# Performance work log

Measured on AMD Instinct MI355X. Metric: run time of the kernel, lower is better.

## Reference

```python
import jax, jax.numpy as jnp
import numpy as np

N_NODES = 50000
N_EDGES = 800000
N_LABELS = 50      # len(deplabel2idx) == len(deplabels)
EMB = 64           # dep_emb_size
HID = 96           # dep_hidden_dim


def _glorot(key, shape):
    fan_in, fan_out = shape
    lim = jnp.sqrt(6.0 / (fan_in + fan_out)).astype(jnp.float32)
    return jax.random.uniform(key, shape, jnp.float32, -lim, lim)


def setup_inputs() -> dict:
    key = jax.random.key(0)
    ks = jax.random.split(key, 10)
    dep_labels = jax.random.randint(ks[0], (N_NODES,), 0, N_LABELS)
    src = jax.random.randint(ks[1], (N_EDGES,), 0, N_NODES)
    dst = jax.random.randint(ks[2], (N_EDGES,), 0, N_NODES)
    emb = jax.random.normal(ks[3], (N_LABELS, EMB), jnp.float32)
    W1 = _glorot(ks[4], (EMB, HID)); b1 = jnp.zeros((HID,), jnp.float32)
    W2 = _glorot(ks[5], (HID, HID)); b2 = jnp.zeros((HID,), jnp.float32)
    W3 = _glorot(ks[6], (HID, N_LABELS)); b3 = jnp.zeros((N_LABELS,), jnp.float32)
    return {"dep_labels": dep_labels, "src": src, "dst": dst, "emb": emb,
            "W1": W1, "b1": b1, "W2": W2, "b2": b2, "W3": W3, "b3": b3}


def _graph_conv(h, src, dst, out_norm, in_norm, W, b, relu):
    # DGL GraphConv norm='both': D_out^{-1/2} scaling at src, sum-aggregate
    # over incoming edges, D_in^{-1/2} scaling at dst, then linear (+ act).
    m = (h * out_norm[:, None])[src]                      # [E, d]
    agg = jax.ops.segment_sum(m, dst, num_segments=h.shape[0])
    agg = agg * in_norm[:, None]                          # [N, d]
    out = agg @ W + b
    return jax.nn.relu(out) if relu else out


def reference(dep_labels, src, dst, emb, W1, b1, W2, b2, W3, b3):
    n = emb.shape[1] * 0 + N_NODES
    ones = jnp.ones((src.shape[0],), jnp.float32)
    out_deg = jax.ops.segment_sum(ones, src, num_segments=N_NODES)
    in_deg = jax.ops.segment_sum(ones, dst, num_segments=N_NODES)
    out_norm = jax.lax.rsqrt(jnp.maximum(out_deg, 1.0))
    in_norm = jax.lax.rsqrt(jnp.maximum(in_deg, 1.0))
    h = emb[dep_labels]                                   # embedding lookup [N, EMB]
    # dropout p=0.0 between layers -> identity (eval-mode reference)
    h = _graph_conv(h, src, dst, out_norm, in_norm, W1, b1, relu=True)
    h = _graph_conv(h, src, dst, out_norm, in_norm, W2, b2, relu=True)
    h = _graph_conv(h, src, dst, out_norm, in_norm, W3, b3, relu=False)
    return h
```

## Files before the change

### kernel.cpp

```cpp
#include <hip/hip_runtime.h>
#include <hip/hip_fp16.h>

#define N_NODES 50000
#define N_EDGES 800000
#define EMB     64
#define HID     96
#define NLAB    50
#define NB_SCAN ((N_NODES + 255) / 256)
#define TSTRIDE 64
#define TC      13
#define T1B     ((NLAB * HID + 255) / 256)
#define NBP     256
#define EPB     ((N_EDGES + NBP - 1) / NBP)
#define NBUCK   196
#define WSTRIDE 104
#define WPREP_N (160 * WSTRIDE)
#define WPREPB  ((WPREP_N + 255) / 256)
#define NMFMA   ((N_NODES + 127) / 128)

typedef _Float16 f16x8 __attribute__((ext_vector_type(8)));
typedef float f32x4 __attribute__((ext_vector_type(4)));

__device__ __forceinline__ float2 h2f(unsigned u) {
    __half2 h = *reinterpret_cast<__half2*>(&u);
    return __half22float2(h);
}
__device__ __forceinline__ unsigned f2h(float a, float b) {
    __half2 h = __floats2half2_rn(a, b);
    return *reinterpret_cast<unsigned*>(&h);
}

__global__ void coarse_hist_kernel(const int* __restrict__ src, const int* __restrict__ dst,
                                   int* __restrict__ histd, int* __restrict__ hists,
                                   const float* __restrict__ emb, const float* __restrict__ W1,
                                   float* __restrict__ T1,
                                   const float* __restrict__ W2, const float* __restrict__ W3,
                                   __half* __restrict__ wprep) {
    int b = blockIdx.x, t = threadIdx.x;
    if (b < NBP) {
        __shared__ int hd[256], hs[256];
        hd[t] = 0; hs[t] = 0;
        __syncthreads();
        int hi = min(b * EPB + EPB, N_EDGES);
        for (int i = b * EPB + t; i < hi; i += 256) {
            atomicAdd(&hd[((unsigned)dst[i]) >> 8], 1);
            atomicAdd(&hs[((unsigned)src[i]) >> 8], 1);
        }
        __syncthreads();
        histd[b * 256 + t] = hd[t];
        hists[b * 256 + t] = hs[t];
    } else if (b < NBP + T1B) {
        int i = (b - NBP) * 256 + t;
        if (i < NLAB * HID) {
            int l = i / HID, j = i - l * HID;
            float sum = 0.0f;
#pragma unroll
            for (int k = 0; k < EMB; ++k) sum += emb[l * EMB + k] * W1[k * HID + j];
            T1[i] = sum;
        }
    } else {
        int i = (b - NBP - T1B) * 256 + t;
        if (i < WPREP_N) {
            int j = i / WSTRIDE, kk = i - j * WSTRIDE;
            float v = 0.0f;
            if (kk < HID) {
                if (j < HID) v = W2[kk * HID + j];
                else { int jj = j - HID; if (jj < NLAB) v = W3[kk * NLAB + jj]; }
            }
            wprep[i] = __float2half(v);
        }
    }
}

__global__ void coarse_scan_kernel(const int* __restrict__ histd, const int* __restrict__ hists,
                                   int* __restrict__ blkrel_d, int* __restrict__ blkrel_s,
                                   int* __restrict__ bbase_d, int* __restrict__ bbase_s) {
    __shared__ int sh[256];
    int t = threadIdx.x;
    const int* hist = blockIdx.x ? hists : histd;
    int* blkrel     = blockIdx.x ? blkrel_s : blkrel_d;
    int* bbase      = blockIdx.x ? bbase_s : bbase_d;
    int run = 0;
#pragma unroll 16
    for (int b = 0; b < NBP; ++b) {
        blkrel[b * 256 + t] = run;
        run += hist[b * 256 + t];
    }
    sh[t] = run;
    __syncthreads();
    for (int off = 1; off < 256; off <<= 1) {
        int v = sh[t];
        if (t >= off) v += sh[t - off];
        __syncthreads();
        sh[t] = v;
        __syncthreads();
    }
    bbase[t] = sh[t] - run;
}

__global__ void partition_kernel(const int* __restrict__ src, const int* __restrict__ dst,
                                 const int* __restrict__ blkrel_d, const int* __restrict__ blkrel_s,
                                 const int* __restrict__ bbase_d, const int* __restrict__ bbase_s,
                                 int* __restrict__ dstp, unsigned char* __restrict__ srcp) {
    __shared__ int curd[256], curs[256];
    int b = blockIdx.x, t = threadIdx.x;
    curd[t] = bbase_d[t] + blkrel_d[b * 256 + t];
    curs[t] = bbase_s[t] + blkrel_s[b * 256 + t];
    __syncthreads();
    int hi = min(b * EPB + EPB, N_EDGES);
    for (int i = b * EPB + t; i < hi; i += 256) {
        int d = dst[i], s = src[i];
        int pd = atomicAdd(&curd[((unsigned)d) >> 8], 1);
        dstp[pd] = s | ((d & 0xFF) << 16);
        int ps = atomicAdd(&curs[((unsigned)s) >> 8], 1);
        srcp[ps] = (unsigned char)(s & 0xFF);
    }
}

__global__ void fine_hist_kernel(const int* __restrict__ dstp, const unsigned char* __restrict__ srcp,
                                 const int* __restrict__ bbase_d, const int* __restrict__ bbase_s,
                                 const int* __restrict__ labels,
                                 int* __restrict__ deg_in, int* __restrict__ deg_out,
                                 float* __restrict__ out_norm, int2* __restrict__ node_info,
                                 int* __restrict__ bsum) {
    __shared__ int cnt[256];
    int b = blockIdx.x, t = threadIdx.x;
    cnt[t] = 0;
    __syncthreads();
    if (b < NBUCK) {
        int lo = bbase_d[b], hi = bbase_d[b + 1];
        for (int i = lo + t; i < hi; i += 256)
            atomicAdd(&cnt[(dstp[i] >> 16) & 0xFF], 1);
        __syncthreads();
        int node = b * 256 + t;
        if (node < N_NODES) deg_in[node] = cnt[t];
        for (int off = 128; off > 0; off >>= 1) {
            __syncthreads();
            if (t < off) cnt[t] += cnt[t + off];
        }
        if (t == 0) bsum[b] = cnt[0];
    } else {
        int bb = b - NBUCK;
        int lo = bbase_s[bb], hi = bbase_s[bb + 1];
        for (int i = lo + t; i < hi; i += 256)
            atomicAdd(&cnt[srcp[i]], 1);
        __syncthreads();
        int node = bb * 256 + t;
        if (node < N_NODES) {
            int d = cnt[t];
            deg_out[node] = d;
            float on = rsqrtf(fmaxf((float)d, 1.0f));
            out_norm[node] = on;
            node_info[node] = make_int2(labels[node] << 16, __float_as_int(on));
        }
    }
}

__global__ void scan_scatter_kernel(const int* __restrict__ deg_in, const int* __restrict__ bsum,
                                    const int* __restrict__ dstp, const int* __restrict__ bbase_d,
                                    const int2* __restrict__ node_info,
                                    int* __restrict__ row_off, float* __restrict__ in_norm,
                                    int2* __restrict__ edge_rec) {
    __shared__ int pb[256];
    __shared__ int s[256];
    __shared__ int ro[256];
    __shared__ int cur[256];
    int t = threadIdx.x, b = blockIdx.x, i = b * 256 + t;
    pb[t] = (t < b) ? bsum[t] : 0;
    int own = (i < N_NODES) ? deg_in[i] : 0;
    s[t] = own;
    cur[t] = 0;
    __syncthreads();
    for (int off = 128; off > 0; off >>= 1) {
        if (t < off) pb[t] += pb[t + off];
        __syncthreads();
    }
    int base = pb[0];
    for (int off = 1; off < 256; off <<= 1) {
        int v = s[t];
        if (t >= off) v += s[t - off];
        __syncthreads();
        s[t] = v;
        __syncthreads();
    }
    int r0 = base + s[t] - own;
    ro[t] = r0;
    if (i < N_NODES) {
        row_off[i] = r0;
        in_norm[i] = rsqrtf(fmaxf((float)own, 1.0f));
    }
    __syncthreads();
    int lo = bbase_d[b], hi = bbase_d[b + 1];
    for (int k = lo + t; k < hi; k += 256) {
        int rec = dstp[k];
        int sn = rec & 0xFFFF;
        int nl = (rec >> 16) & 0xFF;
        int r = atomicAdd(&cur[nl], 1);
        int2 ni = node_info[sn];
        edge_rec[ro[nl] + r] = make_int2(sn | ni.x, ni.y);
    }
}

__global__ void gather1t_kernel(const int2* __restrict__ edge_rec, const float* __restrict__ T1,
                                const int* __restrict__ row_off, const int* __restrict__ deg,
                                const float* __restrict__ in_norm,
                                const float* __restrict__ out_norm, const float* __restrict__ b1,
                                __half* __restrict__ h1s) {
    constexpr int C = HID / 8;
    int i = blockIdx.x * blockDim.x + threadIdx.x;
    if (i >= N_NODES * C) return;
    int n = i / C;
    int c = i - n * C;
    const float* t1a = T1 + c * 4;
    const float* t1b = T1 + (c + C) * 4;
    int k = row_off[n];
    int e = k + deg[n];
    float ax = 0.f, ay = 0.f, az = 0.f, aw = 0.f;
    float bx = 0.f, by = 0.f, bz = 0.f, bw = 0.f;
    for (; k + 3 < e; k += 4) {
        int2 i0 = edge_rec[k];
        int2 i1 = edge_rec[k + 1];
        int2 i2 = edge_rec[k + 2];
        int2 i3 = edge_rec[k + 3];
        int r0 = ((unsigned)i0.x >> 16) * HID, r1 = ((unsigned)i1.x >> 16) * HID;
        int r2 = ((unsigned)i2.x >> 16) * HID, r3 = ((unsigned)i3.x >> 16) * HID;
        float4 aA = *(const float4*)(t1a + r0); float4 bA = *(const float4*)(t1b + r0);
        float4 aB = *(const float4*)(t1a + r1); float4 bB = *(const float4*)(t1b + r1);
        float4 aC = *(const float4*)(t1a + r2); float4 bC = *(const float4*)(t1b + r2);
        float4 aD = *(const float4*)(t1a + r3); float4 bD = *(const float4*)(t1b + r3);
        float w0 = __int_as_float(i0.y), w1 = __int_as_float(i1.y);
        float w2 = __int_as_float(i2.y), w3 = __int_as_float(i3.y);
        ax += aA.x * w0 + aB.x * w1 + aC.x * w2 + aD.x * w3;
        ay += aA.y * w0 + aB.y * w1 + aC.y * w2 + aD.y * w3;
        az += aA.z * w0 + aB.z * w1 + aC.z * w2 + aD.z * w3;
        aw += aA.w * w0 + aB.w * w1 + aC.w * w2 + aD.w * w3;
        bx += bA.x * w0 + bB.x * w1 + bC.x * w2 + bD.x * w3;
        by += bA.y * w0 + bB.y * w1 + bC.y * w2 + bD.y * w3;
        bz += bA.z * w0 + bB.z * w1 + bC.z * w2 + bD.z * w3;
        bw += bA.w * w0 + bB.w * w1 + bC.w * w2 + bD.w * w3;
    }
    for (; k < e; ++k) {
        int2 i0 = edge_rec[k];
        int r0 = ((unsigned)i0.x >> 16) * HID;
        float4 aA = *(const float4*)(t1a + r0); float4 bA = *(const float4*)(t1b + r0);
        float w0 = __int_as_float(i0.y);
        ax += aA.x * w0; ay += aA.y * w0; az += aA.z * w0; aw += aA.w * w0;
        bx += bA.x * w0; by += bA.y * w0; bz += bA.z * w0; bw += bA.w * w0;
    }
    float nn = in_norm[n];
    float on = out_norm[n];
    float4 b1a = *(const float4*)(b1 + c * 4);
    float4 b1b = *(const float4*)(b1 + (c + C) * 4);
    uint2 rA, rB;
    rA.x = f2h(fmaxf(ax * nn + b1a.x, 0.f) * on, fmaxf(ay * nn + b1a.y, 0.f) * on);
    rA.y = f2h(fmaxf(az * nn + b1a.z, 0.f) * on, fmaxf(aw * nn + b1a.w, 0.f) * on);
    rB.x = f2h(fmaxf(bx * nn + b1b.x, 0.f) * on, fmaxf(by * nn + b1b.y, 0.f) * on);
    rB.y = f2h(fmaxf(bz * nn + b1b.z, 0.f) * on, fmaxf(bw * nn + b1b.w, 0.f) * on);
    __half* op = h1s + (size_t)n * HID;
    *(uint2*)(op + c * 4) = rA;
    *(uint2*)(op + (c + C) * 4) = rB;
}

__global__ __launch_bounds__(512) void agg_linear23_kernel(
        const __half* __restrict__ hs, const int* __restrict__ row_off,
        const int* __restrict__ deg, const int2* __restrict__ erec,
        const float* __restrict__ in_norm, const __half* __restrict__ wprep,
        const float* __restrict__ b2, const float* __restrict__ out_norm,
        __half* __restrict__ t) {
    __shared__ _Float16 Wl[WPREP_N];
    __shared__ _Float16 A[128][WSTRIDE];
    const int tid = threadIdx.x;
    {
        const uint4* sp = (const uint4*)wprep;
        uint4* dp = (uint4*)Wl;
        for (int i = tid; i < WPREP_N / 8; i += 512) dp[i] = sp[i];
    }
    const int n0b = blockIdx.x * 128;

    for (int task = tid; task < 128 * 12; task += 512) {
        int m = task / 12;
        int c = task - m * 12;
        int n = n0b + m;
        uint2 rA = make_uint2(0u, 0u), rB = make_uint2(0u, 0u);
        if (n < N_NODES) {
            const __half* p0 = hs + c * 4;
            const __half* p1 = hs + (c + 12) * 4;
            int k = row_off[n];
            int e = k + deg[n];
            float ax = 0.f, ay = 0.f, az = 0.f, aw = 0.f;
            float bx = 0.f, by = 0.f, bz = 0.f, bw = 0.f;
            for (; k + 3 < e; k += 4) {
                size_t r0 = (size_t)(erec[k].x & 0xFFFF) * HID;
                size_t r1 = (size_t)(erec[k + 1].x & 0xFFFF) * HID;
                size_t r2 = (size_t)(erec[k + 2].x & 0xFFFF) * HID;
                size_t r3 = (size_t)(erec[k + 3].x & 0xFFFF) * HID;
                uint2 aA = *(const uint2*)(p0 + r0); uint2 bA = *(const uint2*)(p1 + r0);
                uint2 aB = *(const uint2*)(p0 + r1); uint2 bB = *(const uint2*)(p1 + r1);
                uint2 aC = *(const uint2*)(p0 + r2); uint2 bC = *(const uint2*)(p1 + r2);
                uint2 aD = *(const uint2*)(p0 + r3); uint2 bD = *(const uint2*)(p1 + r3);
                float2 f;
                f = h2f(aA.x); ax += f.x; ay += f.y;  f = h2f(aA.y); az += f.x; aw += f.y;
                f = h2f(aB.x); ax += f.x; ay += f.y;  f = h2f(aB.y); az += f.x; aw += f.y;
                f = h2f(aC.x); ax += f.x; ay += f.y;  f = h2f(aC.y); az += f.x; aw += f.y;
                f = h2f(aD.x); ax += f.x; ay += f.y;  f = h2f(aD.y); az += f.x; aw += f.y;
                f = h2f(bA.x); bx += f.x; by += f.y;  f = h2f(bA.y); bz += f.x; bw += f.y;
                f = h2f(bB.x); bx += f.x; by += f.y;  f = h2f(bB.y); bz += f.x; bw += f.y;
                f = h2f(bC.x); bx += f.x; by += f.y;  f = h2f(bC.y); bz += f.x; bw += f.y;
                f = h2f(bD.x); bx += f.x; by += f.y;  f = h2f(bD.y); bz += f.x; bw += f.y;
            }
            for (; k < e; ++k) {
                size_t r0 = (size_t)(erec[k].x & 0xFFFF) * HID;
                uint2 aA = *(const uint2*)(p0 + r0); uint2 bA = *(const uint2*)(p1 + r0);
                float2 f;
                f = h2f(aA.x); ax += f.x; ay += f.y;  f = h2f(aA.y); az += f.x; aw += f.y;
                f = h2f(bA.x); bx += f.x; by += f.y;  f = h2f(bA.y); bz += f.x; bw += f.y;
            }
            float nn = in_norm[n];
            rA.x = f2h(ax * nn, ay * nn); rA.y = f2h(az * nn, aw * nn);
            rB.x = f2h(bx * nn, by * nn); rB.y = f2h(bz * nn, bw * nn);
        }
        *(uint2*)(&A[m][c * 4]) = rA;
        *(uint2*)(&A[m][(c + 12) * 4]) = rB;
    }
    __syncthreads();

    const int w = tid >> 6, l = tid & 63;
    const int lr = l & 15, lg = l >> 4;
    const int m0 = w * 16;
    const int n0 = n0b + m0;

    f16x8 a[3];
#pragma unroll
    for (int kb = 0; kb < 3; ++kb)
        a[kb] = *(const f16x8*)(&A[m0 + lr][kb * 32 + lg * 8]);
    f32x4 acc[6];
#pragma unroll
    for (int nt = 0; nt < 6; ++nt) {
        acc[nt] = (f32x4){0.f, 0.f, 0.f, 0.f};
#pragma unroll
        for (int kb = 0; kb < 3; ++kb) {
            f16x8 bfr = *(const f16x8*)(&Wl[(nt * 16 + lr) * WSTRIDE + kb * 32 + lg * 8]);
            acc[nt] = __builtin_amdgcn_mfma_f32_16x16x32_f16(a[kb], bfr, acc[nt], 0, 0, 0);
        }
    }
    float on4[4];
#pragma unroll
    for (int r = 0; r < 4; ++r) {
        int n = n0 + lg * 4 + r; if (n > N_NODES - 1) n = N_NODES - 1;
        on4[r] = out_norm[n];
    }
    asm volatile("s_waitcnt lgkmcnt(0)" ::: "memory");
#pragma unroll
    for (int nt = 0; nt < 6; ++nt) {
        int col = nt * 16 + lr;
        float bb = b2[col];
#pragma unroll
        for (int r = 0; r < 4; ++r) {
            float v = fmaxf(acc[nt][r] + bb, 0.f) * on4[r];
            A[m0 + lg * 4 + r][col] = (_Float16)v;
        }
    }
    asm volatile("s_waitcnt lgkmcnt(0)" ::: "memory");

    f16x8 a2[3];
#pragma unroll
    for (int kb = 0; kb < 3; ++kb)
        a2[kb] = *(const f16x8*)(&A[m0 + lr][kb * 32 + lg * 8]);
#pragma unroll
    for (int nt = 0; nt < 4; ++nt) {
        f32x4 acc2 = (f32x4){0.f, 0.f, 0.f, 0.f};
#pragma unroll
        for (int kb = 0; kb < 3; ++kb) {
            f16x8 bfr = *(const f16x8*)(&Wl[(HID + nt * 16 + lr) * WSTRIDE + kb * 32 + lg * 8]);
            acc2 = __builtin_amdgcn_mfma_f32_16x16x32_f16(a2[kb], bfr, acc2, 0, 0, 0);
        }
        int col = nt * 16 + lr;
        if (col < 4 * TC) {
#pragma unroll
            for (int r = 0; r < 4; ++r) {
                int n = n0 + lg * 4 + r;
                if (n < N_NODES) t[(size_t)n * TSTRIDE + col] = __float2half(acc2[r]);
            }
        }
    }
}

__global__ void gather_out_kernel(const __half* __restrict__ t, const int* __restrict__ row_off,
                                  const int* __restrict__ deg, const int2* __restrict__ erec,
                                  const float* __restrict__ in_norm, const float* __restrict__ bias,
                                  float* __restrict__ out) {
    int i = blockIdx.x * blockDim.x + threadIdx.x;
    if (i >= N_NODES * TC) return;
    int n = i / TC;
    int c = i - n * TC;
    const __half* p0 = t + c * 4;
    int k = row_off[n];
    int e = k + deg[n];
    float ax = 0.f, ay = 0.f, az = 0.f, aw = 0.f;
    for (; k + 3 < e; k += 4) {
        size_t r0 = (size_t)(erec[k].x & 0xFFFF) * TSTRIDE;
        size_t r1 = (size_t)(erec[k + 1].x & 0xFFFF) * TSTRIDE;
        size_t r2 = (size_t)(erec[k + 2].x & 0xFFFF) * TSTRIDE;
        size_t r3 = (size_t)(erec[k + 3].x & 0xFFFF) * TSTRIDE;
        uint2 v0 = *(const uint2*)(p0 + r0);
        uint2 v1 = *(const uint2*)(p0 + r1);
        uint2 v2 = *(const uint2*)(p0 + r2);
        uint2 v3 = *(const uint2*)(p0 + r3);
        float2 f;
        f = h2f(v0.x); ax += f.x; ay += f.y;  f = h2f(v0.y); az += f.x; aw += f.y;
        f = h2f(v1.x); ax += f.x; ay += f.y;  f = h2f(v1.y); az += f.x; aw += f.y;
        f = h2f(v2.x); ax += f.x; ay += f.y;  f = h2f(v2.y); az += f.x; aw += f.y;
        f = h2f(v3.x); ax += f.x; ay += f.y;  f = h2f(v3.y); az += f.x; aw += f.y;
    }
    for (; k < e; ++k) {
        size_t r0 = (size_t)(erec[k].x & 0xFFFF) * TSTRIDE;
        uint2 v0 = *(const uint2*)(p0 + r0);
        float2 f;
        f = h2f(v0.x); ax += f.x; ay += f.y;  f = h2f(v0.y); az += f.x; aw += f.y;
    }
    float nn = in_norm[n];
    int j = c * 4;
    float* op = out + (size_t)n * NLAB + j;
    float2 lo; lo.x = ax * nn + bias[j];     lo.y = ay * nn + bias[j + 1];
    *(float2*)op = lo;
    if (j + 2 < NLAB) {
        float2 hi; hi.x = az * nn + bias[j + 2]; hi.y = aw * nn + bias[j + 3];
        *(float2*)(op + 2) = hi;
    }
}

static inline int cdiv(long a, int b) { return (int)((a + b - 1) / b); }

extern "C" void kernel_launch(void* const* d_in, const int* in_sizes, int n_in,
                              void* d_out, int out_size, void* d_ws, size_t ws_size,
                              hipStream_t stream) {
    const int*   dep_labels = (const int*)d_in[0];
    const int*   src        = (const int*)d_in[1];
    const int*   dst        = (const int*)d_in[2];
    const float* emb        = (const float*)d_in[3];
    const float* W1 = (const float*)d_in[4]; const float* b1 = (const float*)d_in[5];
    const float* W2 = (const float*)d_in[6]; const float* b2 = (const float*)d_in[7];
    const float* W3 = (const float*)d_in[8]; const float* b3 = (const float*)d_in[9];
    float* out = (float*)d_out;

    int* wsp           = (int*)d_ws;
    int* row_off       = wsp;                 wsp += N_NODES;
    int* deg_in        = wsp;                 wsp += N_NODES;
    int* deg_out_a     = wsp;                 wsp += N_NODES;
    int* bsum          = wsp;                 wsp += 256;
    float* out_norm    = (float*)wsp;         wsp += N_NODES;
    float* in_norm     = (float*)wsp;         wsp += N_NODES;
    int2* node_info    = (int2*)wsp;          wsp += 2 * N_NODES;
    float* T1          = (float*)wsp;         wsp += NLAB * HID + 16;
    __half* wprep      = (__half*)wsp;        wsp += WPREP_N / 2;
    int2* edge_rec     = (int2*)wsp;          wsp += 2 * N_EDGES;
    int* bufA          = wsp;                 wsp += (size_t)N_NODES * HID;
    __half* bufH       = (__half*)wsp;
    __half* tbuf       = (__half*)bufA;
    int* histd    = bufA;
    int* hists    = histd + NBP * 256;
    int* blkrel_d = hists + NBP * 256;
    int* blkrel_s = blkrel_d + NBP * 256;
    int* bbase_d  = blkrel_s + NBP * 256;
    int* bbase_s  = bbase_d + 256;
    int* dstp     = bbase_s + 256;
    unsigned char* srcp = (unsigned char*)(dstp + N_EDGES);

    const int B = 256;

    coarse_hist_kernel<<<NBP + T1B + WPREPB, B, 0, stream>>>(src, dst, histd, hists,
                                                             emb, W1, T1, W2, W3, wprep);
    coarse_scan_kernel<<<2, B, 0, stream>>>(histd, hists, blkrel_d, blkrel_s, bbase_d, bbase_s);
    partition_kernel<<<NBP, B, 0, stream>>>(src, dst, blkrel_d, blkrel_s, bbase_d, bbase_s,
                                            dstp, srcp);
    fine_hist_kernel<<<2 * NBUCK, B, 0, stream>>>(dstp, srcp, bbase_d, bbase_s, dep_labels,
                                                  deg_in, deg_out_a, out_norm, node_info, bsum);
    scan_scatter_kernel<<<NBUCK, B, 0, stream>>>(deg_in, bsum, dstp, bbase_d, node_info,
                                                 row_off, in_norm, edge_rec);

    gather1t_kernel<<<cdiv((long)N_NODES * (HID / 8), B), B, 0, stream>>>(
        edge_rec, T1, row_off, deg_in, in_norm, out_norm, b1, bufH);

    agg_linear23_kernel<<<NMFMA, 512, 0, stream>>>(
        bufH, row_off, deg_in, edge_rec, in_norm, wprep, b2, out_norm, tbuf);

    gather_out_kernel<<<cdiv((long)N_NODES * TC, B), B, 0, stream>>>(
        tbuf, row_off, deg_in, edge_rec, in_norm, b3, out);
}
```

Measured before the change: 200.6 us.

## Replace layer-1 gather with per-node label histogram times T1 via MFMA

Layer 1 is rewritten algebraically. Because input features are label embeddings, scan_scatter now accumulates, for each destination node, a 50-bin histogram of out_norm-weighted source labels in shared memory. A new MFMA kernel multiplies that histogram by the fp16 emb@W1 table to produce h1. This replaces the per-edge 96-wide gather. Edge records shrink from int2 to 16-bit source ids for the later gathers, which cuts index bandwidth. The cost is a 50KB shared histogram per block with float atomics, an extra S buffer write and read, and fp16 rounding of the histogram and T1.

```diff
diff --git a/kernel.cpp b/kernel.cpp
--- a/kernel.cpp
+++ b/kernel.cpp
@@ -6,16 +6,18 @@
 #define EMB     64
 #define HID     96
 #define NLAB    50
-#define NB_SCAN ((N_NODES + 255) / 256)
 #define TSTRIDE 64
 #define TC      13
-#define T1B     ((NLAB * HID + 255) / 256)
 #define NBP     256
 #define EPB     ((N_EDGES + NBP - 1) / NBP)
 #define NBUCK   196
 #define WSTRIDE 104
 #define WPREP_N (160 * WSTRIDE)
 #define WPREPB  ((WPREP_N + 255) / 256)
+#define T1TSTR  72
+#define T1T_N   (HID * T1TSTR)
+#define T1TB    ((T1T_N + 255) / 256)
+#define SSTR    64
 #define NMFMA   ((N_NODES + 127) / 128)
 
 typedef _Float16 f16x8 __attribute__((ext_vector_type(8)));
@@ -33,7 +35,7 @@
 __global__ void coarse_hist_kernel(const int* __restrict__ src, const int* __restrict__ dst,
                                    int* __restrict__ histd, int* __restrict__ hists,
                                    const float* __restrict__ emb, const float* __restrict__ W1,
-                                   float* __restrict__ T1,
+                                   __half* __restrict__ T1t,
                                    const float* __restrict__ W2, const float* __restrict__ W3,
                                    __half* __restrict__ wprep) {
     int b = blockIdx.x, t = threadIdx.x;
@@ -49,17 +51,19 @@
         __syncthreads();
         histd[b * 256 + t] = hd[t];
         hists[b * 256 + t] = hs[t];
-    } else if (b < NBP + T1B) {
+    } else if (b < NBP + T1TB) {
         int i = (b - NBP) * 256 + t;
-        if (i < NLAB * HID) {
-            int l = i / HID, j = i - l * HID;
+        if (i < T1T_N) {
+            int j = i / T1TSTR, l = i - j * T1TSTR;
             float sum = 0.0f;
-#pragma unroll
-            for (int k = 0; k < EMB; ++k) sum += emb[l * EMB + k] * W1[k * HID + j];
-            T1[i] = sum;
+            if (l < NLAB) {
+#pragma unroll
+                for (int m = 0; m < EMB; ++m) sum += emb[l * EMB + m] * W1[m * HID + j];
+            }
+            T1t[i] = __float2half(sum);
         }
     } else {
-        int i = (b - NBP - T1B) * 256 + t;
+        int i = (b - NBP - T1TB) * 256 + t;
         if (i < WPREP_N) {
             int j = i / WSTRIDE, kk = i - j * WSTRIDE;
             float v = 0.0f;
@@ -160,12 +164,14 @@
                                     const int* __restrict__ dstp, const int* __restrict__ bbase_d,
                                     const int2* __restrict__ node_info,
                                     int* __restrict__ row_off, float* __restrict__ in_norm,
-                                    int2* __restrict__ edge_rec) {
+                                    unsigned short* __restrict__ esrc, float* __restrict__ S) {
     __shared__ int pb[256];
     __shared__ int s[256];
     __shared__ int ro[256];
     __shared__ int cur[256];
+    __shared__ float Sl[256][NLAB];
     int t = threadIdx.x, b = blockIdx.x, i = b * 256 + t;
+    for (int idx = t; idx < 256 * NLAB; idx += 256) ((float*)Sl)[idx] = 0.0f;
     pb[t] = (t < b) ? bsum[t] : 0;
     int own = (i < N_NODES) ? deg_in[i] : 0;
     s[t] = own;
@@ -196,74 +202,75 @@
         int sn = rec & 0xFFFF;
         int nl = (rec >> 16) & 0xFF;
         int r = atomicAdd(&cur[nl], 1);
+        esrc[ro[nl] + r] = (unsigned short)sn;
         int2 ni = node_info[sn];
-        edge_rec[ro[nl] + r] = make_int2(sn | ni.x, ni.y);
-    }
-}
-
-__global__ void gather1t_kernel(const int2* __restrict__ edge_rec, const float* __restrict__ T1,
-                                const int* __restrict__ row_off, const int* __restrict__ deg,
-                                const float* __restrict__ in_norm,
-                                const float* __restrict__ out_norm, const float* __restrict__ b1,
-                                __half* __restrict__ h1s) {
-    constexpr int C = HID / 8;
-    int i = blockIdx.x * blockDim.x + threadIdx.x;
-    if (i >= N_NODES * C) return;
-    int n = i / C;
-    int c = i - n * C;
-    const float* t1a = T1 + c * 4;
-    const float* t1b = T1 + (c + C) * 4;
-    int k = row_off[n];
-    int e = k + deg[n];
-    float ax = 0.f, ay = 0.f, az = 0.f, aw = 0.f;
-    float bx = 0.f, by = 0.f, bz = 0.f, bw = 0.f;
-    for (; k + 3 < e; k += 4) {
-        int2 i0 = edge_rec[k];
-        int2 i1 = edge_rec[k + 1];
-        int2 i2 = edge_rec[k + 2];
-        int2 i3 = edge_rec[k + 3];
-        int r0 = ((unsigned)i0.x >> 16) * HID, r1 = ((unsigned)i1.x >> 16) * HID;
-        int r2 = ((unsigned)i2.x >> 16) * HID, r3 = ((unsigned)i3.x >> 16) * HID;
-        float4 aA = *(const float4*)(t1a + r0); float4 bA = *(const float4*)(t1b + r0);
-        float4 aB = *(const float4*)(t1a + r1); float4 bB = *(const float4*)(t1b + r1);
-        float4 aC = *(const float4*)(t1a + r2); float4 bC = *(const float4*)(t1b + r2);
-        float4 aD = *(const float4*)(t1a + r3); float4 bD = *(const float4*)(t1b + r3);
-        float w0 = __int_as_float(i0.y), w1 = __int_as_float(i1.y);
-        float w2 = __int_as_float(i2.y), w3 = __int_as_float(i3.y);
-        ax += aA.x * w0 + aB.x * w1 + aC.x * w2 + aD.x * w3;
-        ay += aA.y * w0 + aB.y * w1 + aC.y * w2 + aD.y * w3;
-        az += aA.z * w0 + aB.z * w1 + aC.z * w2 + aD.z * w3;
-        aw += aA.w * w0 + aB.w * w1 + aC.w * w2 + aD.w * w3;
-        bx += bA.x * w0 + bB.x * w1 + bC.x * w2 + bD.x * w3;
-        by += bA.y * w0 + bB.y * w1 + bC.y * w2 + bD.y * w3;
-        bz += bA.z * w0 + bB.z * w1 + bC.z * w2 + bD.z * w3;
-        bw += bA.w * w0 + bB.w * w1 + bC.w * w2 + bD.w * w3;
-    }
-    for (; k < e; ++k) {
-        int2 i0 = edge_rec[k];
-        int r0 = ((unsigned)i0.x >> 16) * HID;
-        float4 aA = *(const float4*)(t1a + r0); float4 bA = *(const float4*)(t1b + r0);
-        float w0 = __int_as_float(i0.y);
-        ax += aA.x * w0; ay += aA.y * w0; az += aA.z * w0; aw += aA.w * w0;
-        bx += bA.x * w0; by += bA.y * w0; bz += bA.z * w0; bw += bA.w * w0;
-    }
-    float nn = in_norm[n];
-    float on = out_norm[n];
-    float4 b1a = *(const float4*)(b1 + c * 4);
-    float4 b1b = *(const float4*)(b1 + (c + C) * 4);
-    uint2 rA, rB;
-    rA.x = f2h(fmaxf(ax * nn + b1a.x, 0.f) * on, fmaxf(ay * nn + b1a.y, 0.f) * on);
-    rA.y = f2h(fmaxf(az * nn + b1a.z, 0.f) * on, fmaxf(aw * nn + b1a.w, 0.f) * on);
-    rB.x = f2h(fmaxf(bx * nn + b1b.x, 0.f) * on, fmaxf(by * nn + b1b.y, 0.f) * on);
-    rB.y = f2h(fmaxf(bz * nn + b1b.z, 0.f) * on, fmaxf(bw * nn + b1b.w, 0.f) * on);
-    __half* op = h1s + (size_t)n * HID;
-    *(uint2*)(op + c * 4) = rA;
-    *(uint2*)(op + (c + C) * 4) = rB;
+        atomicAdd(&Sl[nl][((unsigned)ni.x) >> 16], __int_as_float(ni.y));
+    }
+    __syncthreads();
+    for (int idx = t; idx < 256 * SSTR; idx += 256) {
+        int n = idx >> 6, c = idx & 63;
+        int node = b * 256 + n;
+        if (node < N_NODES)
+            S[(size_t)node * SSTR + c] = (c < NLAB) ? Sl[n][c] : 0.0f;
+    }
+}
+
+__global__ __launch_bounds__(512) void h1_mfma_kernel(
+        const float* __restrict__ S, const __half* __restrict__ T1t,
+        const float* __restrict__ b1, const float* __restrict__ in_norm,
+        const float* __restrict__ out_norm, __half* __restrict__ h1s) {
+    const int tid = threadIdx.x;
+    const int w = tid >> 6, l = tid & 63;
+    const int lr = l & 15, lg = l >> 4;
+    const int n0 = blockIdx.x * 128 + w * 16;
+
+    f16x8 a[2];
+    {
+        int n = n0 + lr; if (n > N_NODES - 1) n = N_NODES - 1;
+        const float* sp = S + (size_t)n * SSTR + lg * 8;
+#pragma unroll
+        for (int kb = 0; kb < 2; ++kb) {
+            float4 v0 = *(const float4*)(sp + kb * 32);
+            float4 v1 = *(const float4*)(sp + kb * 32 + 4);
+            a[kb] = (f16x8){(_Float16)v0.x, (_Float16)v0.y, (_Float16)v0.z, (_Float16)v0.w,
+                            (_Float16)v1.x, (_Float16)v1.y, (_Float16)v1.z, (_Float16)v1.w};
+        }
+    }
+    f32x4 acc[6];
+#pragma unroll
+    for (int nt = 0; nt < 6; ++nt) {
+        acc[nt] = (f32x4){0.f, 0.f, 0.f, 0.f};
+#pragma unroll
+        for (int kb = 0; kb < 2; ++kb) {
+            f16x8 bfr = *(const f16x8*)(T1t + (nt * 16 + lr) * T1TSTR + kb * 32 + lg * 8);
+            acc[nt] = __builtin_amdgcn_mfma_f32_16x16x32_f16(a[kb], bfr, acc[nt], 0, 0, 0);
+        }
+    }
+    float on4[4], in4[4];
+#pragma unroll
+    for (int r = 0; r < 4; ++r) {
+        int n = n0 + lg * 4 + r; if (n > N_NODES - 1) n = N_NODES - 1;
+        on4[r] = out_norm[n];
+        in4[r] = in_norm[n];
+    }
+#pragma unroll
+    for (int nt = 0; nt < 6; ++nt) {
+        int col = nt * 16 + lr;
+        float bb = b1[col];
+#pragma unroll
+        for (int r = 0; r < 4; ++r) {
+            int n = n0 + lg * 4 + r;
+            if (n < N_NODES) {
+                float v = fmaxf(in4[r] * acc[nt][r] + bb, 0.f) * on4[r];
+                h1s[(size_t)n * HID + col] = __float2half(v);
+            }
+        }
+    }
 }
 
 __global__ __launch_bounds__(512) void agg_linear23_kernel(
         const __half* __restrict__ hs, const int* __restrict__ row_off,
-        const int* __restrict__ deg, const int2* __restrict__ erec,
+        const int* __restrict__ deg, const unsigned short* __restrict__ esrc,
         const float* __restrict__ in_norm, const __half* __restrict__ wprep,
         const float* __restrict__ b2, const float* __restrict__ out_norm,
         __half* __restrict__ t) {
@@ -290,10 +297,10 @@
             float ax = 0.f, ay = 0.f, az = 0.f, aw = 0.f;
             float bx = 0.f, by = 0.f, bz = 0.f, bw = 0.f;
             for (; k + 3 < e; k += 4) {
-                size_t r0 = (size_t)(erec[k].x & 0xFFFF) * HID;
-                size_t r1 = (size_t)(erec[k + 1].x & 0xFFFF) * HID;
-                size_t r2 = (size_t)(erec[k + 2].x & 0xFFFF) * HID;
-                size_t r3 = (size_t)(erec[k + 3].x & 0xFFFF) * HID;
+                size_t r0 = (size_t)esrc[k] * HID;
+                size_t r1 = (size_t)esrc[k + 1] * HID;
+                size_t r2 = (size_t)esrc[k + 2] * HID;
+                size_t r3 = (size_t)esrc[k + 3] * HID;
                 uint2 aA = *(const uint2*)(p0 + r0); uint2 bA = *(const uint2*)(p1 + r0);
                 uint2 aB = *(const uint2*)(p0 + r1); uint2 bB = *(const uint2*)(p1 + r1);
                 uint2 aC = *(const uint2*)(p0 + r2); uint2 bC = *(const uint2*)(p1 + r2);
@@ -309,7 +316,7 @@
                 f = h2f(bD.x); bx += f.x; by += f.y;  f = h2f(bD.y); bz += f.x; bw += f.y;
             }
             for (; k < e; ++k) {
-                size_t r0 = (size_t)(erec[k].x & 0xFFFF) * HID;
+                size_t r0 = (size_t)esrc[k] * HID;
                 uint2 aA = *(const uint2*)(p0 + r0); uint2 bA = *(const uint2*)(p1 + r0);
                 float2 f;
                 f = h2f(aA.x); ax += f.x; ay += f.y;  f = h2f(aA.y); az += f.x; aw += f.y;
@@ -386,7 +393,7 @@
 }
 
 __global__ void gather_out_kernel(const __half* __restrict__ t, const int* __restrict__ row_off,
-                                  const int* __restrict__ deg, const int2* __restrict__ erec,
+                                  const int* __restrict__ deg, const unsigned short* __restrict__ esrc,
                                   const float* __restrict__ in_norm, const float* __restrict__ bias,
                                   float* __restrict__ out) {
     int i = blockIdx.x * blockDim.x + threadIdx.x;
@@ -398,10 +405,10 @@
     int e = k + deg[n];
     float ax = 0.f, ay = 0.f, az = 0.f, aw = 0.f;
     for (; k + 3 < e; k += 4) {
-        size_t r0 = (size_t)(erec[k].x & 0xFFFF) * TSTRIDE;
-        size_t r1 = (size_t)(erec[k + 1].x & 0xFFFF) * TSTRIDE;
-        size_t r2 = (size_t)(erec[k + 2].x & 0xFFFF) * TSTRIDE;
-        size_t r3 = (size_t)(erec[k + 3].x & 0xFFFF) * TSTRIDE;
+        size_t r0 = (size_t)esrc[k] * TSTRIDE;
+        size_t r1 = (size_t)esrc[k + 1] * TSTRIDE;
+        size_t r2 = (size_t)esrc[k + 2] * TSTRIDE;
+        size_t r3 = (size_t)esrc[k + 3] * TSTRIDE;
         uint2 v0 = *(const uint2*)(p0 + r0);
         uint2 v1 = *(const uint2*)(p0 + r1);
         uint2 v2 = *(const uint2*)(p0 + r2);
@@ -413,7 +420,7 @@
         f = h2f(v3.x); ax += f.x; ay += f.y;  f = h2f(v3.y); az += f.x; aw += f.y;
     }
     for (; k < e; ++k) {
-        size_t r0 = (size_t)(erec[k].x & 0xFFFF) * TSTRIDE;
+        size_t r0 = (size_t)esrc[k] * TSTRIDE;
         uint2 v0 = *(const uint2*)(p0 + r0);
         float2 f;
         f = h2f(v0.x); ax += f.x; ay += f.y;  f = h2f(v0.y); az += f.x; aw += f.y;
@@ -451,12 +458,13 @@
     float* out_norm    = (float*)wsp;         wsp += N_NODES;
     float* in_norm     = (float*)wsp;         wsp += N_NODES;
     int2* node_info    = (int2*)wsp;          wsp += 2 * N_NODES;
-    float* T1          = (float*)wsp;         wsp += NLAB * HID + 16;
+    __half* T1t        = (__half*)wsp;        wsp += T1T_N / 2 + 8;
     __half* wprep      = (__half*)wsp;        wsp += WPREP_N / 2;
-    int2* edge_rec     = (int2*)wsp;          wsp += 2 * N_EDGES;
+    unsigned short* esrc = (unsigned short*)wsp; wsp += N_EDGES / 2;
     int* bufA          = wsp;                 wsp += (size_t)N_NODES * HID;
     __half* bufH       = (__half*)wsp;
-    __half* tbuf       = (__half*)bufA;
+    __half* tbuf  = (__half*)bufA;
+    float*  Sbuf  = (float*)(bufA + 1600000);
     int* histd    = bufA;
     int* hists    = histd + NBP * 256;
     int* blkrel_d = hists + NBP * 256;
@@ -468,22 +476,21 @@
 
     const int B = 256;
 
-    coarse_hist_kernel<<<NBP + T1B + WPREPB, B, 0, stream>>>(src, dst, histd, hists,
-                                                             emb, W1, T1, W2, W3, wprep);
+    coarse_hist_kernel<<<NBP + T1TB + WPREPB, B, 0, stream>>>(src, dst, histd, hists,
+                                                              emb, W1, T1t, W2, W3, wprep);
     coarse_scan_kernel<<<2, B, 0, stream>>>(histd, hists, blkrel_d, blkrel_s, bbase_d, bbase_s);
     partition_kernel<<<NBP, B, 0, stream>>>(src, dst, blkrel_d, blkrel_s, bbase_d, bbase_s,
                                             dstp, srcp);
     fine_hist_kernel<<<2 * NBUCK, B, 0, stream>>>(dstp, srcp, bbase_d, bbase_s, dep_labels,
                                                   deg_in, deg_out_a, out_norm, node_info, bsum);
     scan_scatter_kernel<<<NBUCK, B, 0, stream>>>(deg_in, bsum, dstp, bbase_d, node_info,
-                                                 row_off, in_norm, edge_rec);
-
-    gather1t_kernel<<<cdiv((long)N_NODES * (HID / 8), B), B, 0, stream>>>(
-        edge_rec, T1, row_off, deg_in, in_norm, out_norm, b1, bufH);
+                                                 row_off, in_norm, esrc, Sbuf);
+
+    h1_mfma_kernel<<<NMFMA, 512, 0, stream>>>(Sbuf, T1t, b1, in_norm, out_norm, bufH);
 
     agg_linear23_kernel<<<NMFMA, 512, 0, stream>>>(
-        bufH, row_off, deg_in, edge_rec, in_norm, wprep, b2, out_norm, tbuf);
+        bufH, row_off, deg_in, esrc, in_norm, wprep, b2, out_norm, tbuf);
 
     gather_out_kernel<<<cdiv((long)N_NODES * TC, B), B, 0, stream>>>(
-        tbuf, row_off, deg_in, edge_rec, in_norm, b3, out);
-}
+        tbuf, row_off, deg_in, esrc, in_norm, b3, out);
+}
```

Result: no change. 198.1 us (-1.3%).
